# Kernel tuning notes

Measured on AMD Instinct MI355X. Metric: run time of the kernel, lower is better.

The kernel has to match this reference:

```python
import jax, jax.numpy as jnp
import numpy as np

# Complex Daubechies 6-tap filters: row 0 = real part, row 1 = imaginary part.
LO = np.array([[-0.0662912607, 0.1104854346, 0.6629126074, 0.6629126074, 0.1104854346, -0.0662912607],
               [-0.0855816496, -0.0855816496, 0.1711632992, 0.1711632992, -0.0855816496, -0.0855816496]], dtype=np.float32)
HI = np.array([[-0.0662912607, -0.1104854346, 0.6629126074, -0.6629126074, 0.1104854346, 0.0662912607],
               [0.0855816496, -0.0855816496, -0.1711632992, 0.1711632992, 0.0855816496, -0.0855816496]], dtype=np.float32)

LEVELS = 6
PAD = 3      # circular padding on each side
TAPS = 6     # filter length


def setup_inputs() -> dict:
    key = jax.random.key(0)
    images = jax.random.normal(key, (8, 3, 1024, 1024), dtype=jnp.float32)
    return {"images": images, "lo_pass": jnp.asarray(LO), "hi_pass": jnp.asarray(HI)}


def _dconv(x, k):
    """Circular-pad by 3 along last axis, 6-tap correlation, keep even outputs.
    Matches F.pad(mode='circular') + F.conv2d(stride=1) + [0:-1:2] slicing.
    x: [..., L] (L even), k: [6] -> [..., L//2]."""
    L = x.shape[-1]
    xp = jnp.concatenate([x[..., -PAD:], x, x[..., :PAD]], axis=-1)   # [..., L+6]
    idx = 2 * jnp.arange(L // 2)[:, None] + jnp.arange(TAPS)[None, :]  # [L//2, 6]
    return jnp.einsum('...jt,t->...j', xp[..., idx], k)


def _complex_dconv(re, im, k):
    """Complex depthwise conv: (re + i*im) * (kr + i*ki) with downsample."""
    kr, ki = k[0], k[1]
    out_re = _dconv(re, kr) - _dconv(im, ki)
    out_im = _dconv(re, ki) + _dconv(im, kr)
    return out_re, out_im


def _decompose(x, lo, hi):
    """One wavelet level. x: [B,C,2,h,w] -> [B,C,2,h,w]."""
    re, im = x[:, :, 0], x[:, :, 1]
    # vertical pass: transpose so filtering runs along h
    re_t, im_t = re.swapaxes(-1, -2), im.swapaxes(-1, -2)   # [B,C,w,h]
    lr, li = _complex_dconv(re_t, im_t, lo)                 # [B,C,w,h//2]
    hr, him = _complex_dconv(re_t, im_t, hi)
    re1 = jnp.concatenate([lr, hr], axis=-1).swapaxes(-1, -2)  # [B,C,h,w]
    im1 = jnp.concatenate([li, him], axis=-1).swapaxes(-1, -2)
    # horizontal pass
    lr2, li2 = _complex_dconv(re1, im1, lo)                 # [B,C,h,w//2]
    hr2, hi2 = _complex_dconv(re1, im1, hi)
    return jnp.stack([jnp.concatenate([lr2, hr2], axis=-1),
                      jnp.concatenate([li2, hi2], axis=-1)], axis=2)


def reference(images, lo_pass, hi_pass):
    """Complex Daubechies wavelet transform (forward decomposition).
    images: [B,C,H,W] -> [B,C,2,H,W] (real/imag wavelet coefficients)."""
    B, C, H, W = images.shape
    lo = lo_pass * (2.0 ** -0.5)
    hi = hi_pass * (2.0 ** -0.5)
    x = jnp.stack([images, jnp.zeros_like(images)], axis=2)  # [B,C,2,H,W]
    result = jnp.zeros_like(x)
    for i in range(LEVELS):
        h, w = H >> i, W >> i
        sub = x[..., :h, :w] if i == 0 else result[..., :h, :w]
        result = result.at[..., :h, :w].set(_decompose(sub, lo, hi))
    return result
```

## Files before the change

### kernel.cpp

```cpp
#include <hip/hip_runtime.h>


#define FULL_H 1024
#define FULL_W 1024
#define BC_TOTAL 24

template<bool HAS_IM, bool HAS_LL>
__global__ __launch_bounds__(256)
void wavelet_level_kernel(const float* __restrict__ src,
                          const float* __restrict__ lo_pass,
                          const float* __restrict__ hi_pass,
                          float* __restrict__ dst,
                          float* __restrict__ ll_out,
                          int h, int w)
{
    const int j   = blockIdx.x;
    const int bc  = blockIdx.y;
    const int tid = threadIdx.x;
    const int h2  = h >> 1, w2 = w >> 1;

    const float sc = 0.70710678118654752440f;
    float lor[6], loi[6], hir[6], hii[6];
#pragma unroll
    for (int t = 0; t < 6; ++t) {
        lor[t] = lo_pass[t]     * sc;
        loi[t] = lo_pass[6 + t] * sc;
        hir[t] = hi_pass[t]     * sc;
        hii[t] = hi_pass[6 + t] * sc;
    }

    __shared__ float s_lr[FULL_W];
    __shared__ float s_li[FULL_W];
    __shared__ float s_hr[FULL_W];
    __shared__ float s_hi[FULL_W];

    const float* srcRe = src + (size_t)bc * (HAS_IM ? 2 : 1) * h * w;
    const float* srcIm = HAS_IM ? (srcRe + (size_t)h * w) : nullptr;

    const int hm = h - 1;
    const float* rrow[6];
    const float* irow[6];
#pragma unroll
    for (int t = 0; t < 6; ++t) {
        const int y = (2 * j - 3 + t + h) & hm;
        rrow[t] = srcRe + (size_t)y * w;
        if (HAS_IM) irow[t] = srcIm + (size_t)y * w;
    }

    for (int cv = tid; cv < (w >> 2); cv += 256) {
        float alr[4] = {0.f,0.f,0.f,0.f};
        float ali[4] = {0.f,0.f,0.f,0.f};
        float ahr[4] = {0.f,0.f,0.f,0.f};
        float ahi[4] = {0.f,0.f,0.f,0.f};
#pragma unroll
        for (int t = 0; t < 6; ++t) {
            const float4 rv = reinterpret_cast<const float4*>(rrow[t])[cv];
            const float rr[4] = {rv.x, rv.y, rv.z, rv.w};
#pragma unroll
            for (int u = 0; u < 4; ++u) {
                alr[u] = fmaf(rr[u], lor[t], alr[u]);
                ali[u] = fmaf(rr[u], loi[t], ali[u]);
                ahr[u] = fmaf(rr[u], hir[t], ahr[u]);
                ahi[u] = fmaf(rr[u], hii[t], ahi[u]);
            }
            if (HAS_IM) {
                const float4 iv = reinterpret_cast<const float4*>(irow[t])[cv];
                const float ii[4] = {iv.x, iv.y, iv.z, iv.w};
#pragma unroll
                for (int u = 0; u < 4; ++u) {
                    alr[u] = fmaf(-ii[u], loi[t], alr[u]);
                    ali[u] = fmaf( ii[u], lor[t], ali[u]);
                    ahr[u] = fmaf(-ii[u], hii[t], ahr[u]);
                    ahi[u] = fmaf( ii[u], hir[t], ahi[u]);
                }
            }
        }
        reinterpret_cast<float4*>(s_lr)[cv] = make_float4(alr[0], alr[1], alr[2], alr[3]);
        reinterpret_cast<float4*>(s_li)[cv] = make_float4(ali[0], ali[1], ali[2], ali[3]);
        reinterpret_cast<float4*>(s_hr)[cv] = make_float4(ahr[0], ahr[1], ahr[2], ahr[3]);
        reinterpret_cast<float4*>(s_hi)[cv] = make_float4(ahi[0], ahi[1], ahi[2], ahi[3]);
    }
    __syncthreads();

    const int wm = w - 1;
    float* dstRe = dst + (size_t)(bc * 2 + 0) * FULL_H * FULL_W;
    float* dstIm = dst + (size_t)(bc * 2 + 1) * FULL_H * FULL_W;
    float* llRe = nullptr;
    float* llIm = nullptr;
    if (HAS_LL) {
        llRe = ll_out + (size_t)bc * 2 * h2 * w2;
        llIm = llRe + (size_t)h2 * w2;
    }

    for (int q = tid; q < w2; q += 256) {
        float vlr[6], vli[6], vhr[6], vhi[6];
#pragma unroll
        for (int t = 0; t < 6; ++t) {
            const int x = (2 * q - 3 + t + w) & wm;
            vlr[t] = s_lr[x]; vli[t] = s_li[x];
            vhr[t] = s_hr[x]; vhi[t] = s_hi[x];
        }
        float c1=0.f,c2=0.f,c3=0.f,c4=0.f,c5=0.f,c6=0.f,c7=0.f,c8=0.f;
        float d1=0.f,d2=0.f,d3=0.f,d4=0.f,d5=0.f,d6=0.f,d7=0.f,d8=0.f;
#pragma unroll
        for (int t = 0; t < 6; ++t) {
            c1 = fmaf(vlr[t], lor[t], c1);
            c2 = fmaf(vli[t], loi[t], c2);
            c3 = fmaf(vlr[t], loi[t], c3);
            c4 = fmaf(vli[t], lor[t], c4);
            c5 = fmaf(vlr[t], hir[t], c5);
            c6 = fmaf(vli[t], hii[t], c6);
            c7 = fmaf(vlr[t], hii[t], c7);
            c8 = fmaf(vli[t], hir[t], c8);
            d1 = fmaf(vhr[t], lor[t], d1);
            d2 = fmaf(vhi[t], loi[t], d2);
            d3 = fmaf(vhr[t], loi[t], d3);
            d4 = fmaf(vhi[t], lor[t], d4);
            d5 = fmaf(vhr[t], hir[t], d5);
            d6 = fmaf(vhi[t], hii[t], d6);
            d7 = fmaf(vhr[t], hii[t], d7);
            d8 = fmaf(vhi[t], hir[t], d8);
        }
        const float oRe0 = c1 - c2;
        const float oIm0 = c3 + c4;
        const int   j2   = j + h2;

        dstRe[(size_t)j  * FULL_W + q]      = oRe0;
        dstRe[(size_t)j  * FULL_W + q + w2] = c5 - c6;
        dstIm[(size_t)j  * FULL_W + q]      = oIm0;
        dstIm[(size_t)j  * FULL_W + q + w2] = c7 + c8;
        dstRe[(size_t)j2 * FULL_W + q]      = d1 - d2;
        dstRe[(size_t)j2 * FULL_W + q + w2] = d5 - d6;
        dstIm[(size_t)j2 * FULL_W + q]      = d3 + d4;
        dstIm[(size_t)j2 * FULL_W + q + w2] = d7 + d8;

        if (HAS_LL) {
            llRe[(size_t)j * w2 + q] = oRe0;
            llIm[(size_t)j * w2 + q] = oIm0;
        }
    }
}

extern "C" void kernel_launch(void* const* d_in, const int* in_sizes, int n_in,
                              void* d_out, int out_size, void* d_ws, size_t ws_size,
                              hipStream_t stream)
{
    const float* images = (const float*)d_in[0];
    const float* lo     = (const float*)d_in[1];
    const float* hi     = (const float*)d_in[2];
    float* out = (float*)d_out;

    float* bufA = (float*)d_ws;
    float* bufB = bufA + (size_t)BC_TOTAL * 2 * 512 * 512;

    const dim3 blk(256);
    wavelet_level_kernel<false, true><<<dim3(512, BC_TOTAL), blk, 0, stream>>>(
        images, lo, hi, out, bufA, 1024, 1024);
    wavelet_level_kernel<true,  true><<<dim3(256, BC_TOTAL), blk, 0, stream>>>(
        bufA,   lo, hi, out, bufB,  512,  512);
    wavelet_level_kernel<true,  true><<<dim3(128, BC_TOTAL), blk, 0, stream>>>(
        bufB,   lo, hi, out, bufA,  256,  256);
    wavelet_level_kernel<true,  true><<<dim3( 64, BC_TOTAL), blk, 0, stream>>>(
        bufA,   lo, hi, out, bufB,  128,  128);
    wavelet_level_kernel<true,  true><<<dim3( 32, BC_TOTAL), blk, 0, stream>>>(
        bufB,   lo, hi, out, bufA,   64,   64);
    wavelet_level_kernel<true, false><<<dim3( 16, BC_TOTAL), blk, 0, stream>>>(
        bufA,   lo, hi, out, nullptr, 32,   32);
}
```

Before: 342.7 us.

## Fuse all wavelet levels into one cooperative persistent kernel with grid sync

```diff
diff --git a/kernel.cpp b/kernel.cpp
--- a/kernel.cpp
+++ b/kernel.cpp
@@ -1,144 +1,179 @@
 #include <hip/hip_runtime.h>
-
-
-#define FULL_H 1024
+#include <hip/hip_cooperative_groups.h>
+
+namespace cg = cooperative_groups;
+
+
 #define FULL_W 1024
 #define BC_TOTAL 24
-
-template<bool HAS_IM, bool HAS_LL>
-__global__ __launch_bounds__(256)
-void wavelet_level_kernel(const float* __restrict__ src,
-                          const float* __restrict__ lo_pass,
-                          const float* __restrict__ hi_pass,
-                          float* __restrict__ dst,
-                          float* __restrict__ ll_out,
-                          int h, int w)
-{
-    const int j   = blockIdx.x;
-    const int bc  = blockIdx.y;
+#define SMAX 1040
+
+struct Filt { float lor[6], loi[6], hir[6], hii[6]; };
+
+__device__ __forceinline__ void load_filters(const float* __restrict__ lo_pass,
+                                             const float* __restrict__ hi_pass,
+                                             Filt& f) {
+    const float sc = 0.70710678118654752440f;
+#pragma unroll
+    for (int t = 0; t < 6; ++t) {
+        f.lor[t] = lo_pass[t]     * sc;
+        f.loi[t] = lo_pass[6 + t] * sc;
+        f.hir[t] = hi_pass[t]     * sc;
+        f.hii[t] = hi_pass[6 + t] * sc;
+    }
+}
+
+template<int PPB, int W, bool HAS_IM, bool LAST>
+__device__ __forceinline__ void run_level(const float* __restrict__ src,
+                                          float* __restrict__ dst,
+                                          float* __restrict__ ll_out,
+                                          const Filt& f,
+                                          float* __restrict__ s_lr,
+                                          float* __restrict__ s_li,
+                                          float* __restrict__ s_hr,
+                                          float* __restrict__ s_hi)
+{
+    constexpr int H    = W;
+    constexpr int W2   = W / 2;
+    constexpr int H2   = H / 2;
+    constexpr int SSTR = W + 8;
+    constexpr int NV   = W / 4;
+    constexpr int GRPS = H2 / PPB;
+    constexpr int UNITS = BC_TOTAL * GRPS;
     const int tid = threadIdx.x;
-    const int h2  = h >> 1, w2 = w >> 1;
-
-    const float sc = 0.70710678118654752440f;
-    float lor[6], loi[6], hir[6], hii[6];
-#pragma unroll
-    for (int t = 0; t < 6; ++t) {
-        lor[t] = lo_pass[t]     * sc;
-        loi[t] = lo_pass[6 + t] * sc;
-        hir[t] = hi_pass[t]     * sc;
-        hii[t] = hi_pass[6 + t] * sc;
-    }
-
-    __shared__ float s_lr[FULL_W];
-    __shared__ float s_li[FULL_W];
-    __shared__ float s_hr[FULL_W];
-    __shared__ float s_hi[FULL_W];
-
-    const float* srcRe = src + (size_t)bc * (HAS_IM ? 2 : 1) * h * w;
-    const float* srcIm = HAS_IM ? (srcRe + (size_t)h * w) : nullptr;
-
-    const int hm = h - 1;
-    const float* rrow[6];
-    const float* irow[6];
-#pragma unroll
-    for (int t = 0; t < 6; ++t) {
-        const int y = (2 * j - 3 + t + h) & hm;
-        rrow[t] = srcRe + (size_t)y * w;
-        if (HAS_IM) irow[t] = srcIm + (size_t)y * w;
-    }
-
-    for (int cv = tid; cv < (w >> 2); cv += 256) {
-        float alr[4] = {0.f,0.f,0.f,0.f};
-        float ali[4] = {0.f,0.f,0.f,0.f};
-        float ahr[4] = {0.f,0.f,0.f,0.f};
-        float ahi[4] = {0.f,0.f,0.f,0.f};
-#pragma unroll
-        for (int t = 0; t < 6; ++t) {
-            const float4 rv = reinterpret_cast<const float4*>(rrow[t])[cv];
-            const float rr[4] = {rv.x, rv.y, rv.z, rv.w};
-#pragma unroll
-            for (int u = 0; u < 4; ++u) {
-                alr[u] = fmaf(rr[u], lor[t], alr[u]);
-                ali[u] = fmaf(rr[u], loi[t], ali[u]);
-                ahr[u] = fmaf(rr[u], hir[t], ahr[u]);
-                ahi[u] = fmaf(rr[u], hii[t], ahi[u]);
-            }
-            if (HAS_IM) {
-                const float4 iv = reinterpret_cast<const float4*>(irow[t])[cv];
-                const float ii[4] = {iv.x, iv.y, iv.z, iv.w};
-#pragma unroll
-                for (int u = 0; u < 4; ++u) {
-                    alr[u] = fmaf(-ii[u], loi[t], alr[u]);
-                    ali[u] = fmaf( ii[u], lor[t], ali[u]);
-                    ahr[u] = fmaf(-ii[u], hii[t], ahr[u]);
-                    ahi[u] = fmaf( ii[u], hir[t], ahi[u]);
+
+    for (int u = blockIdx.x; u < UNITS; u += gridDim.x) {
+        const int bc = u / GRPS;
+        const int g0 = (u % GRPS) * PPB;
+        const float* srcRe = src + (size_t)bc * (HAS_IM ? 2 : 1) * H * W;
+
+        if (tid < PPB * NV) {
+            const int p  = tid / NV;
+            const int cv = tid - p * NV;
+            const int j  = g0 + p;
+            float alr[4] = {0.f,0.f,0.f,0.f};
+            float ali[4] = {0.f,0.f,0.f,0.f};
+            float ahr[4] = {0.f,0.f,0.f,0.f};
+            float ahi[4] = {0.f,0.f,0.f,0.f};
+#pragma unroll
+            for (int t = 0; t < 6; ++t) {
+                const int y = (2*j - 3 + t + H) & (H - 1);
+                const float4 rv = *reinterpret_cast<const float4*>(srcRe + (size_t)y*W + 4*cv);
+                const float rr[4] = {rv.x, rv.y, rv.z, rv.w};
+#pragma unroll
+                for (int k = 0; k < 4; ++k) {
+                    alr[k] = fmaf(rr[k], f.lor[t], alr[k]);
+                    ali[k] = fmaf(rr[k], f.loi[t], ali[k]);
+                    ahr[k] = fmaf(rr[k], f.hir[t], ahr[k]);
+                    ahi[k] = fmaf(rr[k], f.hii[t], ahi[k]);
+                }
+                if constexpr (HAS_IM) {
+                    const float4 iv = *reinterpret_cast<const float4*>(
+                        srcRe + (size_t)H*W + (size_t)y*W + 4*cv);
+                    const float ii[4] = {iv.x, iv.y, iv.z, iv.w};
+#pragma unroll
+                    for (int k = 0; k < 4; ++k) {
+                        alr[k] = fmaf(-ii[k], f.loi[t], alr[k]);
+                        ali[k] = fmaf( ii[k], f.lor[t], ali[k]);
+                        ahr[k] = fmaf(-ii[k], f.hii[t], ahr[k]);
+                        ahi[k] = fmaf( ii[k], f.hir[t], ahi[k]);
+                    }
                 }
             }
+            const int o = p*SSTR + 4 + 4*cv;
+            *reinterpret_cast<float4*>(s_lr + o) = make_float4(alr[0],alr[1],alr[2],alr[3]);
+            *reinterpret_cast<float4*>(s_li + o) = make_float4(ali[0],ali[1],ali[2],ali[3]);
+            *reinterpret_cast<float4*>(s_hr + o) = make_float4(ahr[0],ahr[1],ahr[2],ahr[3]);
+            *reinterpret_cast<float4*>(s_hi + o) = make_float4(ahi[0],ahi[1],ahi[2],ahi[3]);
         }
-        reinterpret_cast<float4*>(s_lr)[cv] = make_float4(alr[0], alr[1], alr[2], alr[3]);
-        reinterpret_cast<float4*>(s_li)[cv] = make_float4(ali[0], ali[1], ali[2], ali[3]);
-        reinterpret_cast<float4*>(s_hr)[cv] = make_float4(ahr[0], ahr[1], ahr[2], ahr[3]);
-        reinterpret_cast<float4*>(s_hi)[cv] = make_float4(ahi[0], ahi[1], ahi[2], ahi[3]);
+        __syncthreads();
+
+        if (tid < PPB * 3) {
+            const int p = tid / 3, k = tid - p * 3, b = p * SSTR;
+            s_lr[b+1+k] = s_lr[b+4+W-3+k];   s_lr[b+4+W+k] = s_lr[b+4+k];
+            s_li[b+1+k] = s_li[b+4+W-3+k];   s_li[b+4+W+k] = s_li[b+4+k];
+            s_hr[b+1+k] = s_hr[b+4+W-3+k];   s_hr[b+4+W+k] = s_hr[b+4+k];
+            s_hi[b+1+k] = s_hi[b+4+W-3+k];   s_hi[b+4+W+k] = s_hi[b+4+k];
+        }
+        __syncthreads();
+
+        float* dstRe = dst + (size_t)(bc*2) * FULL_W * FULL_W;
+        float* dstIm = dstRe + (size_t)FULL_W * FULL_W;
+        for (int qq = tid; qq < PPB * W2; qq += 256) {
+            const int p = qq / W2;
+            const int q = qq - p * W2;
+            const int j = g0 + p;
+            const int bi = p*SSTR + 1 + 2*q;
+            float c1=0.f,c2=0.f,c3=0.f,c4=0.f,c5=0.f,c6=0.f,c7=0.f,c8=0.f;
+            float d1=0.f,d2=0.f,d3=0.f,d4=0.f,d5=0.f,d6=0.f,d7=0.f,d8=0.f;
+#pragma unroll
+            for (int t = 0; t < 6; ++t) {
+                const float vlr = s_lr[bi+t], vli = s_li[bi+t];
+                const float vhr = s_hr[bi+t], vhi = s_hi[bi+t];
+                c1 = fmaf(vlr, f.lor[t], c1);  c2 = fmaf(vli, f.loi[t], c2);
+                c3 = fmaf(vlr, f.loi[t], c3);  c4 = fmaf(vli, f.lor[t], c4);
+                c5 = fmaf(vlr, f.hir[t], c5);  c6 = fmaf(vli, f.hii[t], c6);
+                c7 = fmaf(vlr, f.hii[t], c7);  c8 = fmaf(vli, f.hir[t], c8);
+                d1 = fmaf(vhr, f.lor[t], d1);  d2 = fmaf(vhi, f.loi[t], d2);
+                d3 = fmaf(vhr, f.loi[t], d3);  d4 = fmaf(vhi, f.lor[t], d4);
+                d5 = fmaf(vhr, f.hir[t], d5);  d6 = fmaf(vhi, f.hii[t], d6);
+                d7 = fmaf(vhr, f.hii[t], d7);  d8 = fmaf(vhi, f.hir[t], d8);
+            }
+            const float oRe0 = c1 - c2;
+            const float oIm0 = c3 + c4;
+            const int   j2   = j + H2;
+            __builtin_nontemporal_store(c5 - c6, dstRe + (size_t)j  * FULL_W + W2 + q);
+            __builtin_nontemporal_store(c7 + c8, dstIm + (size_t)j  * FULL_W + W2 + q);
+            __builtin_nontemporal_store(d1 - d2, dstRe + (size_t)j2 * FULL_W + q);
+            __builtin_nontemporal_store(d5 - d6, dstRe + (size_t)j2 * FULL_W + W2 + q);
+            __builtin_nontemporal_store(d3 + d4, dstIm + (size_t)j2 * FULL_W + q);
+            __builtin_nontemporal_store(d7 + d8, dstIm + (size_t)j2 * FULL_W + W2 + q);
+            if constexpr (LAST) {
+                __builtin_nontemporal_store(oRe0, dstRe + (size_t)j * FULL_W + q);
+                __builtin_nontemporal_store(oIm0, dstIm + (size_t)j * FULL_W + q);
+            } else {
+                float* llRe = ll_out + (size_t)bc * 2 * H2 * W2;
+                llRe[(size_t)j * W2 + q]                   = oRe0;
+                llRe[(size_t)H2 * W2 + (size_t)j * W2 + q] = oIm0;
+            }
+        }
+        __syncthreads();
     }
-    __syncthreads();
-
-    const int wm = w - 1;
-    float* dstRe = dst + (size_t)(bc * 2 + 0) * FULL_H * FULL_W;
-    float* dstIm = dst + (size_t)(bc * 2 + 1) * FULL_H * FULL_W;
-    float* llRe = nullptr;
-    float* llIm = nullptr;
-    if (HAS_LL) {
-        llRe = ll_out + (size_t)bc * 2 * h2 * w2;
-        llIm = llRe + (size_t)h2 * w2;
-    }
-
-    for (int q = tid; q < w2; q += 256) {
-        float vlr[6], vli[6], vhr[6], vhi[6];
-#pragma unroll
-        for (int t = 0; t < 6; ++t) {
-            const int x = (2 * q - 3 + t + w) & wm;
-            vlr[t] = s_lr[x]; vli[t] = s_li[x];
-            vhr[t] = s_hr[x]; vhi[t] = s_hi[x];
-        }
-        float c1=0.f,c2=0.f,c3=0.f,c4=0.f,c5=0.f,c6=0.f,c7=0.f,c8=0.f;
-        float d1=0.f,d2=0.f,d3=0.f,d4=0.f,d5=0.f,d6=0.f,d7=0.f,d8=0.f;
-#pragma unroll
-        for (int t = 0; t < 6; ++t) {
-            c1 = fmaf(vlr[t], lor[t], c1);
-            c2 = fmaf(vli[t], loi[t], c2);
-            c3 = fmaf(vlr[t], loi[t], c3);
-            c4 = fmaf(vli[t], lor[t], c4);
-            c5 = fmaf(vlr[t], hir[t], c5);
-            c6 = fmaf(vli[t], hii[t], c6);
-            c7 = fmaf(vlr[t], hii[t], c7);
-            c8 = fmaf(vli[t], hir[t], c8);
-            d1 = fmaf(vhr[t], lor[t], d1);
-            d2 = fmaf(vhi[t], loi[t], d2);
-            d3 = fmaf(vhr[t], loi[t], d3);
-            d4 = fmaf(vhi[t], lor[t], d4);
-            d5 = fmaf(vhr[t], hir[t], d5);
-            d6 = fmaf(vhi[t], hii[t], d6);
-            d7 = fmaf(vhr[t], hii[t], d7);
-            d8 = fmaf(vhi[t], hir[t], d8);
-        }
-        const float oRe0 = c1 - c2;
-        const float oIm0 = c3 + c4;
-        const int   j2   = j + h2;
-
-        dstRe[(size_t)j  * FULL_W + q]      = oRe0;
-        dstRe[(size_t)j  * FULL_W + q + w2] = c5 - c6;
-        dstIm[(size_t)j  * FULL_W + q]      = oIm0;
-        dstIm[(size_t)j  * FULL_W + q + w2] = c7 + c8;
-        dstRe[(size_t)j2 * FULL_W + q]      = d1 - d2;
-        dstRe[(size_t)j2 * FULL_W + q + w2] = d5 - d6;
-        dstIm[(size_t)j2 * FULL_W + q]      = d3 + d4;
-        dstIm[(size_t)j2 * FULL_W + q + w2] = d7 + d8;
-
-        if (HAS_LL) {
-            llRe[(size_t)j * w2 + q] = oRe0;
-            llIm[(size_t)j * w2 + q] = oIm0;
-        }
-    }
+}
+
+__global__ __launch_bounds__(256)
+void wavelet_all(const float* __restrict__ images, const float* __restrict__ lo_pass,
+                 const float* __restrict__ hi_pass, float* __restrict__ out,
+                 float* __restrict__ bufA, float* __restrict__ bufB)
+{
+    __shared__ float s_lr[SMAX], s_li[SMAX], s_hr[SMAX], s_hi[SMAX];
+    Filt f;
+    load_filters(lo_pass, hi_pass, f);
+    cg::grid_group grid = cg::this_grid();
+
+    run_level<1,1024,false,false>(images, out, bufA, f, s_lr,s_li,s_hr,s_hi);
+    __threadfence(); grid.sync();
+    run_level<1, 512,true ,false>(bufA,   out, bufB, f, s_lr,s_li,s_hr,s_hi);
+    __threadfence(); grid.sync();
+    run_level<2, 256,true ,false>(bufB,   out, bufA, f, s_lr,s_li,s_hr,s_hi);
+    __threadfence(); grid.sync();
+    run_level<4, 128,true ,false>(bufA,   out, bufB, f, s_lr,s_li,s_hr,s_hi);
+    __threadfence(); grid.sync();
+    run_level<8,  64,true ,false>(bufB,   out, bufA, f, s_lr,s_li,s_hr,s_hi);
+    __threadfence(); grid.sync();
+    run_level<16, 32,true ,true >(bufA,   out, nullptr, f, s_lr,s_li,s_hr,s_hi);
+}
+
+template<int PPB, int W, bool HAS_IM, bool LAST>
+__global__ __launch_bounds__(256)
+void wavelet_one(const float* __restrict__ src, const float* __restrict__ lo_pass,
+                 const float* __restrict__ hi_pass, float* __restrict__ dst,
+                 float* __restrict__ ll)
+{
+    __shared__ float s_lr[PPB*(W+8)], s_li[PPB*(W+8)], s_hr[PPB*(W+8)], s_hi[PPB*(W+8)];
+    Filt f;
+    load_filters(lo_pass, hi_pass, f);
+    run_level<PPB,W,HAS_IM,LAST>(src, dst, ll, f, s_lr,s_li,s_hr,s_hi);
 }
 
 extern "C" void kernel_launch(void* const* d_in, const int* in_sizes, int n_in,
@@ -148,22 +183,31 @@
     const float* images = (const float*)d_in[0];
     const float* lo     = (const float*)d_in[1];
     const float* hi     = (const float*)d_in[2];
-    float* out = (float*)d_out;
-
+    float* out  = (float*)d_out;
     float* bufA = (float*)d_ws;
     float* bufB = bufA + (size_t)BC_TOTAL * 2 * 512 * 512;
 
-    const dim3 blk(256);
-    wavelet_level_kernel<false, true><<<dim3(512, BC_TOTAL), blk, 0, stream>>>(
-        images, lo, hi, out, bufA, 1024, 1024);
-    wavelet_level_kernel<true,  true><<<dim3(256, BC_TOTAL), blk, 0, stream>>>(
-        bufA,   lo, hi, out, bufB,  512,  512);
-    wavelet_level_kernel<true,  true><<<dim3(128, BC_TOTAL), blk, 0, stream>>>(
-        bufB,   lo, hi, out, bufA,  256,  256);
-    wavelet_level_kernel<true,  true><<<dim3( 64, BC_TOTAL), blk, 0, stream>>>(
-        bufA,   lo, hi, out, bufB,  128,  128);
-    wavelet_level_kernel<true,  true><<<dim3( 32, BC_TOTAL), blk, 0, stream>>>(
-        bufB,   lo, hi, out, bufA,   64,   64);
-    wavelet_level_kernel<true, false><<<dim3( 16, BC_TOTAL), blk, 0, stream>>>(
-        bufA,   lo, hi, out, nullptr, 32,   32);
-}
+    int dev = 0;
+    hipGetDevice(&dev);
+    int cus = 0;
+    hipDeviceGetAttribute(&cus, hipDeviceAttributeMultiprocessorCount, dev);
+    if (cus <= 0) cus = 256;
+    int nb = 0;
+    hipError_t oe = hipOccupancyMaxActiveBlocksPerMultiprocessor(&nb, wavelet_all, 256, 0);
+    if (oe != hipSuccess || nb <= 0) nb = 2;
+    int grid = cus * nb;
+    if (grid > 12288) grid = 12288;
+
+    void* args[] = {(void*)&images, (void*)&lo, (void*)&hi,
+                    (void*)&out, (void*)&bufA, (void*)&bufB};
+    hipError_t le = hipLaunchCooperativeKernel((void*)wavelet_all, dim3(grid), dim3(256),
+                                               args, 0, stream);
+    if (le != hipSuccess) {
+        wavelet_one<1,1024,false,false><<<dim3(12288), dim3(256), 0, stream>>>(images, lo, hi, out, bufA);
+        wavelet_one<1, 512,true ,false><<<dim3( 6144), dim3(256), 0, stream>>>(bufA,   lo, hi, out, bufB);
+        wavelet_one<2, 256,true ,false><<<dim3( 1536), dim3(256), 0, stream>>>(bufB,   lo, hi, out, bufA);
+        wavelet_one<4, 128,true ,false><<<dim3(  384), dim3(256), 0, stream>>>(bufA,   lo, hi, out, bufB);
+        wavelet_one<8,  64,true ,false><<<dim3(   96), dim3(256), 0, stream>>>(bufB,   lo, hi, out, bufA);
+        wavelet_one<16, 32,true ,true ><<<dim3(   24), dim3(256), 0, stream>>>(bufA,   lo, hi, out, nullptr);
+    }
+}
```

Result: slower. 661.8 us (+93.1%).
